# Kernel optimization log

Hardware: AMD Instinct MI355X
Metric: run time of the kernel (lower is better)

The kernel has to match this reference:

```python
import jax, jax.numpy as jnp
import numpy as np

NUM_ENTS = 100000
NUM_RELS2 = 1000  # num_rels * 2
H_DIM = 128
NUM_EDGES = 2000000
RRELU_SLOPE = (1.0 / 8.0 + 1.0 / 3.0) / 2.0  # F.rrelu eval-mode negative slope


def l2_normalize(x, eps=1e-12):
    # F.normalize along last dim
    n = jnp.sqrt(jnp.sum(x * x, axis=-1, keepdims=True))
    return x / jnp.maximum(n, eps)


def setup_inputs() -> dict:
    key = jax.random.key(0)
    ks = jax.random.split(key, 11)
    s = 1.0 / np.sqrt(H_DIM)
    return {
        "ent_emb": jax.random.normal(ks[0], (NUM_ENTS, H_DIM), jnp.float32),
        "rel_emb": jax.random.normal(ks[1], (NUM_RELS2, H_DIM), jnp.float32) * s,
        "his": jax.random.normal(ks[2], (NUM_ENTS, H_DIM), jnp.float32),
        "W_neighbor": jax.random.normal(ks[3], (H_DIM, H_DIM), jnp.float32) * s,
        "W_self": jax.random.normal(ks[4], (H_DIM, H_DIM), jnp.float32) * s,
        "time_gate_weight": jax.random.normal(ks[5], (H_DIM, H_DIM), jnp.float32) * s,
        "time_gate_bias": jnp.zeros((H_DIM,), jnp.float32),
        "edge_norm": jax.random.uniform(ks[6], (NUM_EDGES,), jnp.float32),
        "src": jax.random.randint(ks[7], (NUM_EDGES,), 0, NUM_ENTS, jnp.int32),
        "dst": jax.random.randint(ks[8], (NUM_EDGES,), 0, NUM_ENTS, jnp.int32),
        "etype": jax.random.randint(ks[9], (NUM_EDGES,), 0, NUM_RELS2, jnp.int32),
    }


def reference(ent_emb, rel_emb, his, W_neighbor, W_self, time_gate_weight,
              time_gate_bias, edge_norm, src, dst, etype):
    # layer_norm=True branch: L2-normalize entity embeddings (F.normalize)
    h = l2_normalize(ent_emb)                                   # [N, D]
    # UnionRGCNLayer message: (h[src] + rel_emb[etype]) @ W, scaled by edge norm
    node = h[src] + rel_emb[etype]                              # [E, D] gather
    msg = (node @ W_neighbor) * edge_norm[:, None]              # [E, D]
    agg = jax.ops.segment_sum(msg, dst, num_segments=NUM_ENTS)  # [N, D] scatter
    # self-loop + rrelu (eval mode: leaky with mean slope)
    h_cur = agg + h @ W_self
    h_cur = jnp.where(h_cur >= 0, h_cur, RRELU_SLOPE * h_cur)
    # time gate: blend current with historical embedding
    gate = jax.nn.sigmoid(h_cur @ time_gate_weight + time_gate_bias)
    out = gate * h_cur + (1.0 - gate) * his
    return out
```

## Files before the change

### kernel.cpp

```cpp
#include <hip/hip_runtime.h>
#include <math.h>

#define NUM_ENTS   100000
#define HD         128
#define NUM_EDGES  2000000
#define NUM_RELS2  1000
#define RRELU_SLOPE 0.22916666666666666f
#define NBLK 391
#define NPAD (NBLK * 256)
#define EQ4  (NUM_EDGES / 4)
#define EBLK ((EQ4 + 255) / 256)
#define PBLK ((EQ4 + 511) / 512)

#define SB_HIST EBLK
#define SB_HB   25000
#define SB_RB   125
#define SB_WP   24
#define SB_TOTAL (SB_HIST + SB_HB + SB_RB + SB_WP)

typedef __attribute__((ext_vector_type(8))) short bf16x8;
typedef __attribute__((ext_vector_type(4))) float f32x4;

__device__ __forceinline__ float bf2f(unsigned short h) {
    union { unsigned int u; float f; } v;
    v.u = ((unsigned int)h) << 16;
    return v.f;
}
__device__ __forceinline__ void unpack2(unsigned int u, float& lo, float& hi) {
    union { unsigned int u; float f; } a, b;
    a.u = u << 16;
    b.u = u & 0xffff0000u;
    lo = a.f; hi = b.f;
}
__device__ __forceinline__ unsigned short f2bf(float f) {
    union { float f; unsigned int u; } v; v.f = f;
    unsigned int r = 0x7fffu + ((v.u >> 16) & 1u);
    return (unsigned short)((v.u + r) >> 16);
}

__global__ void __launch_bounds__(256)
setup_kernel(const float* __restrict__ ent, const float* __restrict__ rel,
             const float* __restrict__ Wn, const float* __restrict__ Ws,
             const float* __restrict__ Wt, const int* __restrict__ dst,
             int* __restrict__ cnt, int* __restrict__ pos,
             unsigned short* __restrict__ hb,
             unsigned short* __restrict__ rb, unsigned short* __restrict__ Wp) {
    const int bid = blockIdx.x, tid = threadIdx.x;
    if (bid < SB_HIST) {
        const int i = bid * 256 + tid;
        if (i < EQ4) {
            const int4 d4 = ((const int4*)dst)[i];
            int4 p4;
            p4.x = atomicAdd(&cnt[d4.x], 1);
            p4.y = atomicAdd(&cnt[d4.y], 1);
            p4.z = atomicAdd(&cnt[d4.z], 1);
            p4.w = atomicAdd(&cnt[d4.w], 1);
            ((int4*)pos)[i] = p4;
        }
    } else if (bid < SB_HIST + SB_HB) {
        const int row = (bid - SB_HIST) * 4 + (tid >> 6);
        const int lane = tid & 63;
        const float2 v = *(const float2*)(ent + (size_t)row * HD + lane * 2);
        float ss = v.x * v.x + v.y * v.y;
        #pragma unroll
        for (int m = 1; m < 64; m <<= 1) ss += __shfl_xor(ss, m, 64);
        const float inv = 1.0f / fmaxf(sqrtf(ss), 1e-12f);
        const unsigned int o = (unsigned int)f2bf(v.x * inv) |
                               ((unsigned int)f2bf(v.y * inv) << 16);
        *(unsigned int*)(hb + (size_t)row * HD + lane * 2) = o;
    } else if (bid < SB_HIST + SB_HB + SB_RB) {
        const int i = (bid - SB_HIST - SB_HB) * 256 + tid;
        const float4 v = ((const float4*)rel)[i];
        ushort4 o;
        o.x = f2bf(v.x); o.y = f2bf(v.y); o.z = f2bf(v.z); o.w = f2bf(v.w);
        ((ushort4*)rb)[i] = o;
    } else {
        const int blk = (bid - SB_HIST - SB_HB - SB_RB) * 4 + (tid >> 6);
        const int lane = tid & 63;
        const int w = blk >> 5, rem = blk & 31, t = rem >> 2, kt = rem & 3;
        const float* W = (w == 0) ? Wn : (w == 1) ? Ws : Wt;
        const int n  = t * 16 + (lane & 15);
        const int k0 = kt * 32 + (lane >> 4) * 8;
        unsigned short tmp[8];
        #pragma unroll
        for (int j = 0; j < 8; ++j) tmp[j] = f2bf(W[(size_t)(k0 + j) * HD + n]);
        unsigned short* d = Wp + ((size_t)blk * 64 + lane) * 8;
        *(ushort4*)(d + 0) = make_ushort4(tmp[0], tmp[1], tmp[2], tmp[3]);
        *(ushort4*)(d + 4) = make_ushort4(tmp[4], tmp[5], tmp[6], tmp[7]);
    }
}

__global__ void __launch_bounds__(256)
scan1_kernel(const int* __restrict__ cnt, int* __restrict__ offs, int* __restrict__ bsum) {
    __shared__ int tmp[256];
    const int t = threadIdx.x;
    const int i = blockIdx.x * 256 + t;
    const int v = cnt[i];
    tmp[t] = v;
    __syncthreads();
    #pragma unroll
    for (int d = 1; d < 256; d <<= 1) {
        const int a = (t >= d) ? tmp[t - d] : 0;
        __syncthreads();
        tmp[t] += a;
        __syncthreads();
    }
    offs[i] = tmp[t] - v;
    if (t == 255) bsum[blockIdx.x] = tmp[255];
}

__global__ void __launch_bounds__(512)
scan2_kernel(int* __restrict__ bsum) {
    __shared__ int tmp[512];
    const int t = threadIdx.x;
    const int v = (t < NBLK) ? bsum[t] : 0;
    tmp[t] = v;
    __syncthreads();
    #pragma unroll
    for (int d = 1; d < 512; d <<= 1) {
        const int a = (t >= d) ? tmp[t - d] : 0;
        __syncthreads();
        tmp[t] += a;
        __syncthreads();
    }
    if (t < NBLK) bsum[t] = tmp[t] - v;
}

__global__ void __launch_bounds__(256)
scan3_kernel(int* __restrict__ offs, const int* __restrict__ bsum) {
    const int i = blockIdx.x * 256 + threadIdx.x;
    offs[i] += bsum[blockIdx.x];
}

__global__ void __launch_bounds__(256)
permute_kernel(const int* __restrict__ dst, const int* __restrict__ src,
               const int* __restrict__ ety, const float* __restrict__ enorm,
               const int* __restrict__ offs, const int* __restrict__ pos,
               uint2* __restrict__ recs) {
    #pragma unroll
    for (int u = 0; u < 2; ++u) {
        const int i = blockIdx.x * 512 + u * 256 + threadIdx.x;
        if (i < EQ4) {
            const int4 d4 = ((const int4*)dst)[i];
            const int4 s4 = ((const int4*)src)[i];
            const int4 t4 = ((const int4*)ety)[i];
            const float4 n4 = ((const float4*)enorm)[i];
            const int4 p4 = ((const int4*)pos)[i];
            recs[offs[d4.x] + p4.x] = make_uint2((unsigned int)s4.x | ((unsigned int)t4.x << 17), __float_as_uint(n4.x));
            recs[offs[d4.y] + p4.y] = make_uint2((unsigned int)s4.y | ((unsigned int)t4.y << 17), __float_as_uint(n4.y));
            recs[offs[d4.z] + p4.z] = make_uint2((unsigned int)s4.z | ((unsigned int)t4.z << 17), __float_as_uint(n4.z));
            recs[offs[d4.w] + p4.w] = make_uint2((unsigned int)s4.w | ((unsigned int)t4.w << 17), __float_as_uint(n4.w));
        }
    }
}

__device__ __forceinline__ void accum8(float* acc, uint4 hv, uint4 rv, float w) {
    float h0, h1, r0, r1;
    unpack2(hv.x, h0, h1); unpack2(rv.x, r0, r1);
    acc[0] += (h0 + r0) * w; acc[1] += (h1 + r1) * w;
    unpack2(hv.y, h0, h1); unpack2(rv.y, r0, r1);
    acc[2] += (h0 + r0) * w; acc[3] += (h1 + r1) * w;
    unpack2(hv.z, h0, h1); unpack2(rv.z, r0, r1);
    acc[4] += (h0 + r0) * w; acc[5] += (h1 + r1) * w;
    unpack2(hv.w, h0, h1); unpack2(rv.w, r0, r1);
    acc[6] += (h0 + r0) * w; acc[7] += (h1 + r1) * w;
}

__global__ void __launch_bounds__(256, 4)
gather_mfma(const unsigned short* __restrict__ hb,
            const unsigned short* __restrict__ rb,
            const int* __restrict__ offs,
            const uint2* __restrict__ recs,
            const unsigned short* __restrict__ Wp,
            const float* __restrict__ bias,
            const float* __restrict__ his,
            float* __restrict__ out) {
    __shared__ unsigned short T[16 * 136];
    const int tid = threadIdx.x;
    const int m0 = blockIdx.x * 16;
    const int grp = tid >> 4, sub = tid & 15;
    const int wv = tid >> 6, lane = tid & 63;
    const int rA = lane & 15, quad = lane >> 4;
    const unsigned short* hbp = hb + sub * 8;
    const unsigned short* rbp = rb + sub * 8;

    {
        const int d = m0 + grp;
        const int beg = offs[d], end = offs[d + 1];
        float acc[8] = {0.f, 0.f, 0.f, 0.f, 0.f, 0.f, 0.f, 0.f};
        int i = beg;
        if (i < end) {
            uint2 rcA[4];
            #pragma unroll
            for (int k = 0; k < 4; ++k) rcA[k] = recs[min(i + k, NUM_EDGES - 1)];
            for (; i < end; i += 4) {
                uint2 rcB[4];
                #pragma unroll
                for (int k = 0; k < 4; ++k) rcB[k] = recs[min(i + 4 + k, NUM_EDGES - 1)];
                uint4 hv[4], rv[4]; float w[4];
                #pragma unroll
                for (int k = 0; k < 4; ++k) {
                    w[k] = (i + k) < end ? __uint_as_float(rcA[k].y) : 0.f;
                    hv[k] = *(const uint4*)(hbp + (size_t)(rcA[k].x & 0x1FFFFu) * HD);
                    rv[k] = *(const uint4*)(rbp + (size_t)(rcA[k].x >> 17) * HD);
                }
                #pragma unroll
                for (int k = 0; k < 4; ++k) accum8(acc, hv[k], rv[k], w[k]);
                #pragma unroll
                for (int k = 0; k < 4; ++k) rcA[k] = rcB[k];
            }
        }
        unsigned short* dT = T + grp * 136 + sub * 8;
        *(ushort4*)(dT + 0) = make_ushort4(f2bf(acc[0]), f2bf(acc[1]), f2bf(acc[2]), f2bf(acc[3]));
        *(ushort4*)(dT + 4) = make_ushort4(f2bf(acc[4]), f2bf(acc[5]), f2bf(acc[6]), f2bf(acc[7]));
    }
    __syncthreads();

    const bf16x8* WF = (const bf16x8*)Wp;
    bf16x8 a1[4], a2[4];
    #pragma unroll
    for (int kt = 0; kt < 4; ++kt)
        a1[kt] = *(const bf16x8*)(T + rA * 136 + kt * 32 + quad * 8);
    {
        const unsigned short* base = hb + (size_t)(m0 + rA) * HD + quad * 8;
        #pragma unroll
        for (int kt = 0; kt < 4; ++kt)
            a2[kt] = *(const bf16x8*)(base + kt * 32);
    }

    f32x4 acc1[2];
    #pragma unroll
    for (int tt = 0; tt < 2; ++tt) acc1[tt] = (f32x4)0.f;

    #pragma unroll
    for (int tt = 0; tt < 2; ++tt) {
        const int t = wv * 2 + tt;
        #pragma unroll
        for (int kt = 0; kt < 4; ++kt) {
            const bf16x8 bfr = WF[(size_t)(t * 4 + kt) * 64 + lane];
            acc1[tt] = __builtin_amdgcn_mfma_f32_16x16x32_bf16(a1[kt], bfr, acc1[tt], 0, 0, 0);
        }
        #pragma unroll
        for (int kt = 0; kt < 4; ++kt) {
            const bf16x8 bfr = WF[(size_t)(32 + t * 4 + kt) * 64 + lane];
            acc1[tt] = __builtin_amdgcn_mfma_f32_16x16x32_bf16(a2[kt], bfr, acc1[tt], 0, 0, 0);
        }
    }

    #pragma unroll
    for (int tt = 0; tt < 2; ++tt)
        #pragma unroll
        for (int r = 0; r < 4; ++r)
            acc1[tt][r] = acc1[tt][r] >= 0.f ? acc1[tt][r] : RRELU_SLOPE * acc1[tt][r];

    __syncthreads();
    #pragma unroll
    for (int tt = 0; tt < 2; ++tt)
        #pragma unroll
        for (int r = 0; r < 4; ++r)
            T[(quad * 4 + r) * 136 + (wv * 2 + tt) * 16 + rA] = f2bf(acc1[tt][r]);
    __syncthreads();

    bf16x8 a3[4];
    #pragma unroll
    for (int kt = 0; kt < 4; ++kt)
        a3[kt] = *(const bf16x8*)(T + rA * 136 + kt * 32 + quad * 8);

    #pragma unroll
    for (int tt = 0; tt < 2; ++tt) {
        const int t = wv * 2 + tt;
        const float bn = bias[t * 16 + rA];
        f32x4 c2 = (f32x4){bn, bn, bn, bn};
        #pragma unroll
        for (int kt = 0; kt < 4; ++kt) {
            const bf16x8 bfr = WF[(size_t)(64 + t * 4 + kt) * 64 + lane];
            c2 = __builtin_amdgcn_mfma_f32_16x16x32_bf16(a3[kt], bfr, c2, 0, 0, 0);
        }
        const int col = t * 16 + rA;
        #pragma unroll
        for (int r = 0; r < 4; ++r) {
            const size_t row = (size_t)(m0 + quad * 4 + r);
            const float g = 1.f / (1.f + __expf(-c2[r]));
            const float h = his[row * HD + col];
            out[row * HD + col] = g * acc1[tt][r] + (1.f - g) * h;
        }
    }
}

extern "C" void kernel_launch(void* const* d_in, const int* in_sizes, int n_in,
                              void* d_out, int out_size, void* d_ws, size_t ws_size,
                              hipStream_t stream) {
    const float* ent   = (const float*)d_in[0];
    const float* rel   = (const float*)d_in[1];
    const float* his   = (const float*)d_in[2];
    const float* Wn    = (const float*)d_in[3];
    const float* Ws    = (const float*)d_in[4];
    const float* Wt    = (const float*)d_in[5];
    const float* bias  = (const float*)d_in[6];
    const float* enorm = (const float*)d_in[7];
    const int* src = (const int*)d_in[8];
    const int* dst = (const int*)d_in[9];
    const int* ety = (const int*)d_in[10];
    float* out = (float*)d_out;

    char* p = (char*)d_ws;
    unsigned short* hb = (unsigned short*)p;  p += (size_t)NUM_ENTS * HD * 2;
    unsigned short* rb = (unsigned short*)p;  p += (size_t)NUM_RELS2 * HD * 2;
    unsigned short* Wp = (unsigned short*)p;  p += (size_t)96 * 64 * 8 * 2;
    int* cnt  = (int*)p;                      p += (size_t)NPAD * 4;
    int* offs = (int*)p;                      p += (size_t)NPAD * 4;
    int* bsum = (int*)p;                      p += 512 * 4;
    int* pos  = (int*)p;                      p += (size_t)NUM_EDGES * 4;
    uint2* recs = (uint2*)p;

    hipMemsetAsync(cnt, 0, (size_t)NPAD * 4, stream);
    setup_kernel<<<SB_TOTAL, 256, 0, stream>>>(ent, rel, Wn, Ws, Wt, dst, cnt, pos, hb, rb, Wp);
    scan1_kernel<<<NBLK, 256, 0, stream>>>(cnt, offs, bsum);
    scan2_kernel<<<1, 512, 0, stream>>>(bsum);
    scan3_kernel<<<NBLK, 256, 0, stream>>>(offs, bsum);
    permute_kernel<<<PBLK, 256, 0, stream>>>(dst, src, ety, enorm, offs, pos, recs);
    gather_mfma<<<NUM_ENTS / 16, 256, 0, stream>>>(hb, rb, offs, recs, Wp, bias, his, out);
}
```

Baseline: 411.4 us.

## Merge scan kernels, use wave-shuffle scans, nontemporal loads, packed FMA accumulation

```diff
diff --git a/kernel.cpp b/kernel.cpp
--- a/kernel.cpp
+++ b/kernel.cpp
@@ -20,17 +20,21 @@
 
 typedef __attribute__((ext_vector_type(8))) short bf16x8;
 typedef __attribute__((ext_vector_type(4))) float f32x4;
+typedef __attribute__((ext_vector_type(2))) float f32x2;
+typedef __attribute__((ext_vector_type(2))) unsigned int u32x2;
+typedef __attribute__((ext_vector_type(4))) unsigned int u32x4;
+typedef __attribute__((ext_vector_type(4))) int i32x4;
 
 __device__ __forceinline__ float bf2f(unsigned short h) {
     union { unsigned int u; float f; } v;
     v.u = ((unsigned int)h) << 16;
     return v.f;
 }
-__device__ __forceinline__ void unpack2(unsigned int u, float& lo, float& hi) {
+__device__ __forceinline__ f32x2 up2(unsigned int u) {
     union { unsigned int u; float f; } a, b;
     a.u = u << 16;
     b.u = u & 0xffff0000u;
-    lo = a.f; hi = b.f;
+    return (f32x2){a.f, b.f};
 }
 __device__ __forceinline__ unsigned short f2bf(float f) {
     union { float f; unsigned int u; } v; v.f = f;
@@ -49,13 +53,13 @@
     if (bid < SB_HIST) {
         const int i = bid * 256 + tid;
         if (i < EQ4) {
-            const int4 d4 = ((const int4*)dst)[i];
-            int4 p4;
-            p4.x = atomicAdd(&cnt[d4.x], 1);
-            p4.y = atomicAdd(&cnt[d4.y], 1);
-            p4.z = atomicAdd(&cnt[d4.z], 1);
-            p4.w = atomicAdd(&cnt[d4.w], 1);
-            ((int4*)pos)[i] = p4;
+            const i32x4 d4 = ((const i32x4*)dst)[i];
+            i32x4 p4;
+            p4[0] = atomicAdd(&cnt[d4[0]], 1);
+            p4[1] = atomicAdd(&cnt[d4[1]], 1);
+            p4[2] = atomicAdd(&cnt[d4[2]], 1);
+            p4[3] = atomicAdd(&cnt[d4[3]], 1);
+            ((i32x4*)pos)[i] = p4;
         }
     } else if (bid < SB_HIST + SB_HB) {
         const int row = (bid - SB_HIST) * 4 + (tid >> 6);
@@ -92,85 +96,80 @@
 
 __global__ void __launch_bounds__(256)
 scan1_kernel(const int* __restrict__ cnt, int* __restrict__ offs, int* __restrict__ bsum) {
-    __shared__ int tmp[256];
-    const int t = threadIdx.x;
+    __shared__ int wsum[4];
+    const int t = threadIdx.x, lane = t & 63, wv = t >> 6;
     const int i = blockIdx.x * 256 + t;
     const int v = cnt[i];
-    tmp[t] = v;
-    __syncthreads();
-    #pragma unroll
-    for (int d = 1; d < 256; d <<= 1) {
-        const int a = (t >= d) ? tmp[t - d] : 0;
-        __syncthreads();
-        tmp[t] += a;
-        __syncthreads();
-    }
-    offs[i] = tmp[t] - v;
-    if (t == 255) bsum[blockIdx.x] = tmp[255];
-}
-
-__global__ void __launch_bounds__(512)
-scan2_kernel(int* __restrict__ bsum) {
-    __shared__ int tmp[512];
-    const int t = threadIdx.x;
-    const int v = (t < NBLK) ? bsum[t] : 0;
-    tmp[t] = v;
-    __syncthreads();
-    #pragma unroll
-    for (int d = 1; d < 512; d <<= 1) {
-        const int a = (t >= d) ? tmp[t - d] : 0;
-        __syncthreads();
-        tmp[t] += a;
-        __syncthreads();
-    }
-    if (t < NBLK) bsum[t] = tmp[t] - v;
+    int s = v;
+    #pragma unroll
+    for (int d = 1; d < 64; d <<= 1) {
+        const int u = __shfl_up(s, d, 64);
+        if (lane >= d) s += u;
+    }
+    if (lane == 63) wsum[wv] = s;
+    __syncthreads();
+    int p = 0;
+    #pragma unroll
+    for (int w = 0; w < 3; ++w) p += (w < wv) ? wsum[w] : 0;
+    offs[i] = p + s - v;
+    if (t == 255) bsum[blockIdx.x] = p + s;
 }
 
 __global__ void __launch_bounds__(256)
-scan3_kernel(int* __restrict__ offs, const int* __restrict__ bsum) {
-    const int i = blockIdx.x * 256 + threadIdx.x;
-    offs[i] += bsum[blockIdx.x];
+scanB_kernel(int* __restrict__ offs, const int* __restrict__ bsum) {
+    __shared__ int red[4];
+    const int b = blockIdx.x;
+    const int t = threadIdx.x, lane = t & 63, wv = t >> 6;
+    int v = 0;
+    if (t < b) v = bsum[t];
+    if (t + 256 < b) v += bsum[t + 256];
+    #pragma unroll
+    for (int m = 1; m < 64; m <<= 1) v += __shfl_xor(v, m, 64);
+    if (lane == 0) red[wv] = v;
+    __syncthreads();
+    const int pre = red[0] + red[1] + red[2] + red[3];
+    offs[b * 256 + t] += pre;
 }
 
 __global__ void __launch_bounds__(256)
 permute_kernel(const int* __restrict__ dst, const int* __restrict__ src,
                const int* __restrict__ ety, const float* __restrict__ enorm,
                const int* __restrict__ offs, const int* __restrict__ pos,
-               uint2* __restrict__ recs) {
+               u32x2* __restrict__ recs) {
     #pragma unroll
     for (int u = 0; u < 2; ++u) {
         const int i = blockIdx.x * 512 + u * 256 + threadIdx.x;
         if (i < EQ4) {
-            const int4 d4 = ((const int4*)dst)[i];
-            const int4 s4 = ((const int4*)src)[i];
-            const int4 t4 = ((const int4*)ety)[i];
-            const float4 n4 = ((const float4*)enorm)[i];
-            const int4 p4 = ((const int4*)pos)[i];
-            recs[offs[d4.x] + p4.x] = make_uint2((unsigned int)s4.x | ((unsigned int)t4.x << 17), __float_as_uint(n4.x));
-            recs[offs[d4.y] + p4.y] = make_uint2((unsigned int)s4.y | ((unsigned int)t4.y << 17), __float_as_uint(n4.y));
-            recs[offs[d4.z] + p4.z] = make_uint2((unsigned int)s4.z | ((unsigned int)t4.z << 17), __float_as_uint(n4.z));
-            recs[offs[d4.w] + p4.w] = make_uint2((unsigned int)s4.w | ((unsigned int)t4.w << 17), __float_as_uint(n4.w));
-        }
-    }
-}
-
-__device__ __forceinline__ void accum8(float* acc, uint4 hv, uint4 rv, float w) {
-    float h0, h1, r0, r1;
-    unpack2(hv.x, h0, h1); unpack2(rv.x, r0, r1);
-    acc[0] += (h0 + r0) * w; acc[1] += (h1 + r1) * w;
-    unpack2(hv.y, h0, h1); unpack2(rv.y, r0, r1);
-    acc[2] += (h0 + r0) * w; acc[3] += (h1 + r1) * w;
-    unpack2(hv.z, h0, h1); unpack2(rv.z, r0, r1);
-    acc[4] += (h0 + r0) * w; acc[5] += (h1 + r1) * w;
-    unpack2(hv.w, h0, h1); unpack2(rv.w, r0, r1);
-    acc[6] += (h0 + r0) * w; acc[7] += (h1 + r1) * w;
+            const i32x4 d4 = __builtin_nontemporal_load(&((const i32x4*)dst)[i]);
+            const i32x4 s4 = __builtin_nontemporal_load(&((const i32x4*)src)[i]);
+            const i32x4 t4 = __builtin_nontemporal_load(&((const i32x4*)ety)[i]);
+            const f32x4 n4 = __builtin_nontemporal_load(&((const f32x4*)enorm)[i]);
+            const i32x4 p4 = __builtin_nontemporal_load(&((const i32x4*)pos)[i]);
+            #pragma unroll
+            for (int k = 0; k < 4; ++k) {
+                u32x2 rc;
+                rc[0] = (unsigned int)s4[k] | ((unsigned int)t4[k] << 17);
+                union { float f; unsigned int u; } nb; nb.f = n4[k];
+                rc[1] = nb.u;
+                recs[offs[d4[k]] + p4[k]] = rc;
+            }
+        }
+    }
+}
+
+__device__ __forceinline__ void accum8(f32x2* acc, uint4 hv, uint4 rv, float w) {
+    const f32x2 w2 = (f32x2){w, w};
+    acc[0] = __builtin_elementwise_fma(up2(hv.x) + up2(rv.x), w2, acc[0]);
+    acc[1] = __builtin_elementwise_fma(up2(hv.y) + up2(rv.y), w2, acc[1]);
+    acc[2] = __builtin_elementwise_fma(up2(hv.z) + up2(rv.z), w2, acc[2]);
+    acc[3] = __builtin_elementwise_fma(up2(hv.w) + up2(rv.w), w2, acc[3]);
 }
 
 __global__ void __launch_bounds__(256, 4)
 gather_mfma(const unsigned short* __restrict__ hb,
             const unsigned short* __restrict__ rb,
             const int* __restrict__ offs,
-            const uint2* __restrict__ recs,
+            const u32x2* __restrict__ recs,
             const unsigned short* __restrict__ Wp,
             const float* __restrict__ bias,
             const float* __restrict__ his,
@@ -187,22 +186,27 @@
     {
         const int d = m0 + grp;
         const int beg = offs[d], end = offs[d + 1];
-        float acc[8] = {0.f, 0.f, 0.f, 0.f, 0.f, 0.f, 0.f, 0.f};
+        f32x2 acc[4];
+        #pragma unroll
+        for (int j = 0; j < 4; ++j) acc[j] = (f32x2)0.f;
         int i = beg;
         if (i < end) {
-            uint2 rcA[4];
+            u32x2 rcA[4];
             #pragma unroll
-            for (int k = 0; k < 4; ++k) rcA[k] = recs[min(i + k, NUM_EDGES - 1)];
+            for (int k = 0; k < 4; ++k)
+                rcA[k] = __builtin_nontemporal_load(&recs[min(i + k, NUM_EDGES - 1)]);
             for (; i < end; i += 4) {
-                uint2 rcB[4];
+                u32x2 rcB[4];
                 #pragma unroll
-                for (int k = 0; k < 4; ++k) rcB[k] = recs[min(i + 4 + k, NUM_EDGES - 1)];
+                for (int k = 0; k < 4; ++k)
+                    rcB[k] = __builtin_nontemporal_load(&recs[min(i + 4 + k, NUM_EDGES - 1)]);
                 uint4 hv[4], rv[4]; float w[4];
                 #pragma unroll
                 for (int k = 0; k < 4; ++k) {
-                    w[k] = (i + k) < end ? __uint_as_float(rcA[k].y) : 0.f;
-                    hv[k] = *(const uint4*)(hbp + (size_t)(rcA[k].x & 0x1FFFFu) * HD);
-                    rv[k] = *(const uint4*)(rbp + (size_t)(rcA[k].x >> 17) * HD);
+                    union { unsigned int u; float f; } wb; wb.u = rcA[k][1];
+                    w[k] = (i + k) < end ? wb.f : 0.f;
+                    hv[k] = *(const uint4*)(hbp + (size_t)(rcA[k][0] & 0x1FFFFu) * HD);
+                    rv[k] = *(const uint4*)(rbp + (size_t)(rcA[k][0] >> 17) * HD);
                 }
                 #pragma unroll
                 for (int k = 0; k < 4; ++k) accum8(acc, hv[k], rv[k], w[k]);
@@ -211,8 +215,10 @@
             }
         }
         unsigned short* dT = T + grp * 136 + sub * 8;
-        *(ushort4*)(dT + 0) = make_ushort4(f2bf(acc[0]), f2bf(acc[1]), f2bf(acc[2]), f2bf(acc[3]));
-        *(ushort4*)(dT + 4) = make_ushort4(f2bf(acc[4]), f2bf(acc[5]), f2bf(acc[6]), f2bf(acc[7]));
+        *(ushort4*)(dT + 0) = make_ushort4(f2bf(acc[0][0]), f2bf(acc[0][1]),
+                                           f2bf(acc[1][0]), f2bf(acc[1][1]));
+        *(ushort4*)(dT + 4) = make_ushort4(f2bf(acc[2][0]), f2bf(acc[2][1]),
+                                           f2bf(acc[3][0]), f2bf(acc[3][1]));
     }
     __syncthreads();
 
@@ -281,8 +287,9 @@
         for (int r = 0; r < 4; ++r) {
             const size_t row = (size_t)(m0 + quad * 4 + r);
             const float g = 1.f / (1.f + __expf(-c2[r]));
-            const float h = his[row * HD + col];
-            out[row * HD + col] = g * acc1[tt][r] + (1.f - g) * h;
+            const float h = __builtin_nontemporal_load(his + row * HD + col);
+            __builtin_nontemporal_store(g * acc1[tt][r] + (1.f - g) * h,
+                                        out + row * HD + col);
         }
     }
 }
@@ -311,13 +318,12 @@
     int* offs = (int*)p;                      p += (size_t)NPAD * 4;
     int* bsum = (int*)p;                      p += 512 * 4;
     int* pos  = (int*)p;                      p += (size_t)NUM_EDGES * 4;
-    uint2* recs = (uint2*)p;
+    u32x2* recs = (u32x2*)p;
 
     hipMemsetAsync(cnt, 0, (size_t)NPAD * 4, stream);
     setup_kernel<<<SB_TOTAL, 256, 0, stream>>>(ent, rel, Wn, Ws, Wt, dst, cnt, pos, hb, rb, Wp);
     scan1_kernel<<<NBLK, 256, 0, stream>>>(cnt, offs, bsum);
-    scan2_kernel<<<1, 512, 0, stream>>>(bsum);
-    scan3_kernel<<<NBLK, 256, 0, stream>>>(offs, bsum);
+    scanB_kernel<<<NBLK, 256, 0, stream>>>(offs, bsum);
     permute_kernel<<<PBLK, 256, 0, stream>>>(dst, src, ety, enorm, offs, pos, recs);
     gather_mfma<<<NUM_ENTS / 16, 256, 0, stream>>>(hb, rb, offs, recs, Wp, bias, his, out);
 }
```

Result: slower. 446.3 us (+8.5%).
